# Optimization experiments

Hardware: AMD Instinct MI355X
Metric: run time of the kernel (lower is better)

Reference implementation:

```python
import jax, jax.numpy as jnp
import numpy as np

N = 16384
E = 524288
C = 16

def setup_inputs() -> dict:
    key = jax.random.key(0)
    ks = jax.random.split(key, 8)
    x = jax.random.normal(ks[0], (N, N), dtype=jnp.float32)
    edge_index = jax.random.randint(ks[1], (2, E), 0, N, dtype=jnp.int64)
    def glorot(k, fi, fo):
        s = jnp.sqrt(6.0 / (fi + fo)).astype(jnp.float32)
        return jax.random.uniform(k, (fi, fo), jnp.float32, -s, s)
    return {
        "x": x,
        "edge_index": edge_index,
        "W1": glorot(ks[2], N, 64),  "b1": jnp.zeros((64,), jnp.float32),
        "W2": glorot(ks[3], 64, 32), "b2": jnp.zeros((32,), jnp.float32),
        "W3": glorot(ks[4], 32, C),  "b3": jnp.zeros((C,), jnp.float32),
    }

def _gcn_norm(edge_index, n):
    # add self loops, compute symmetric normalization (PyG gcn_norm)
    loops = jnp.arange(n, dtype=edge_index.dtype)
    row = jnp.concatenate([edge_index[0], loops])  # source
    col = jnp.concatenate([edge_index[1], loops])  # target (aggregation index)
    deg = jax.ops.segment_sum(jnp.ones_like(col, dtype=jnp.float32), col, num_segments=n)
    dis = jnp.where(deg > 0, jax.lax.rsqrt(deg), 0.0)
    norm = dis[row] * dis[col]  # [E+N]
    return row, col, norm

def _gcn_conv(h, row, col, norm, W, b, n):
    h = h @ W                              # [N, F_out]
    msg = h[row] * norm[:, None]           # gather + scale per edge
    out = jax.ops.segment_sum(msg, col, num_segments=n)  # scatter-add at targets
    return out + b

def reference(x, edge_index, W1, b1, W2, b2, W3, b3):
    n = x.shape[0]
    row, col, norm = _gcn_norm(edge_index, n)
    h = jax.nn.relu(_gcn_conv(x, row, col, norm, W1, b1, n))
    h = jax.nn.relu(_gcn_conv(h, row, col, norm, W2, b2, n))
    h = _gcn_conv(h, row, col, norm, W3, b3, n)
    return jax.nn.softmax(h, axis=1)
```

## Files before the change

### kernel.cpp

```cpp
#include <hip/hip_runtime.h>


typedef __attribute__((ext_vector_type(8))) short bf16x8;
typedef __attribute__((ext_vector_type(4))) float f32x4;
typedef __attribute__((ext_vector_type(4))) float fv4;

__device__ __forceinline__ float4 ldnt4(const float* p) {
    fv4 v = __builtin_nontemporal_load((const fv4*)p);
    return make_float4(v.x, v.y, v.z, v.w);
}
__device__ __forceinline__ void stnt(float* p, float v) {
    __builtin_nontemporal_store(v, p);
}

__device__ __forceinline__ unsigned cvt_pk_bf16(float a, float b) {
    unsigned r;
    asm("v_cvt_pk_bf16_f32 %0, %1, %2" : "=v"(r) : "v"(a), "v"(b));
    return r;
}

__device__ __forceinline__ void lds_barrier() {
    asm volatile("s_waitcnt lgkmcnt(0)" ::: "memory");
    __builtin_amdgcn_s_barrier();
    asm volatile("" ::: "memory");
}

__device__ __forceinline__ unsigned short f2bf_rne(float f) {
    unsigned u = __float_as_uint(f);
    unsigned r = (u + 0x7FFFu + ((u >> 16) & 1u)) >> 16;
    return (unsigned short)r;
}

__global__ void init_prep_k(const int* __restrict__ ei, int* __restrict__ flag,
                            int* __restrict__ cnt, int n,
                            const float* __restrict__ W1,
                            unsigned short* __restrict__ Bt, int K) {
    int t = blockIdx.x * blockDim.x + threadIdx.x;
    if (t < n) cnt[t] = 0;
    if (t == 0) {
        int f = 1;
        for (int i = 0; i < 256; ++i) {
            if (ei[2 * i + 1] != 0) { f = 0; break; }
        }
        *flag = f;
    }
    if (t < K * 64) {
        int nn = t & 63, k = t >> 6;
        float f = W1[(size_t)k * 64 + nn];
        unsigned short hi = f2bf_rne(f);
        float hf = __uint_as_float((unsigned)hi << 16);
        unsigned short lo = f2bf_rne(f - hf);
        Bt[(size_t)nn * K + k] = hi;
        Bt[(size_t)64 * K + (size_t)nn * K + k] = lo;
    }
}

__device__ __forceinline__ int edge_val(const int* __restrict__ ei, long long idx, int f64) {
    return f64 ? ei[2 * idx] : ei[(int)idx];
}

__global__ void count_deg_k(const int* __restrict__ ei, int E, const int* __restrict__ flag,
                            int* __restrict__ cnt) {
    int e = blockIdx.x * blockDim.x + threadIdx.x;
    if (e >= E) return;
    int f = *flag;
    int c = edge_val(ei, (long long)E + e, f);
    atomicAdd(&cnt[c], 1);
}

__global__ void scan_blk_k(const int* __restrict__ cnt, int* __restrict__ offs,
                           float* __restrict__ dis, int* __restrict__ cursor,
                           int* __restrict__ btot, int n) {
    __shared__ int sh[256];
    const int t = threadIdx.x;
    const int idx = blockIdx.x * 256 + t;
    int v = (idx < n) ? cnt[idx] : 0;
    sh[t] = v;
    __syncthreads();
    for (int o = 1; o < 256; o <<= 1) {
        int add = (t >= o) ? sh[t - o] : 0;
        __syncthreads();
        sh[t] += add;
        __syncthreads();
    }
    if (idx < n) {
        offs[idx] = sh[t] - v;
        cursor[idx] = 0;
        dis[idx] = rsqrtf((float)(v + 1));
    }
    if (t == 255) btot[blockIdx.x] = sh[255];
}

__global__ void scan_add_k(int* __restrict__ offs, const int* __restrict__ btot,
                           int n, int nb) {
    __shared__ int base_sh, tot_sh;
    const int t = threadIdx.x;
    if (t == 0) {
        int base = 0, tot = 0;
        for (int i = 0; i < nb; ++i) {
            int v = btot[i];
            if (i < (int)blockIdx.x) base += v;
            tot += v;
        }
        base_sh = base;
        tot_sh = tot;
    }
    __syncthreads();
    int idx = blockIdx.x * 256 + t;
    if (idx < n) offs[idx] += base_sh;
    if (blockIdx.x == 0 && t == 0) offs[n] = tot_sh;
}

__global__ void fill_csr_k(const int* __restrict__ ei, int E, const int* __restrict__ flag,
                           const int* __restrict__ offs, int* __restrict__ cursor,
                           const float* __restrict__ dis, int* __restrict__ src,
                           float* __restrict__ w) {
    int e = blockIdx.x * blockDim.x + threadIdx.x;
    if (e >= E) return;
    int f = *flag;
    int r = edge_val(ei, (long long)e, f);
    int c = edge_val(ei, (long long)E + e, f);
    int pos = offs[c] + atomicAdd(&cursor[c], 1);
    src[pos] = r;
    w[pos] = dis[r] * dis[c];
}

__global__ __launch_bounds__(256) void gemm1_mfma_k(
    const float* __restrict__ A, const unsigned short* __restrict__ Bt,
    float* __restrict__ P, int n, int K, int kchunk) {
    __shared__ unsigned short As[2][128][40];
    const int tid = threadIdx.x;
    const int lane = tid & 63;
    const int wid = tid >> 6;
    const int wm = wid >> 1, wn = wid & 1;
    const int lrow = lane & 15, lkh = lane >> 4;
    const int bid = blockIdx.x;
    const int by = (bid & 7) >> 1;
    const int bx = ((bid >> 3) << 1) | (bid & 1);
    const int bm = bx * 128;
    const int k0 = by * kchunk;
    const int iters = kchunk / 32;

    const unsigned short* Bh = Bt;
    const unsigned short* Bl = Bt + (size_t)64 * K;

    f32x4 acc[4][2] = {};
    float4 st[4];

    auto loadA = [&](int kt) {
#pragma unroll
        for (int i = 0; i < 4; ++i) {
            int v = tid + i * 256;
            int r = v >> 3, c = (v & 7) * 4;
            st[i] = ldnt4(A + (size_t)(bm + r) * K + k0 + kt * 32 + c);
        }
    };

    loadA(0);
    for (int kt = 0; kt < iters; ++kt) {
        bf16x8 bh[2], bl[2];
#pragma unroll
        for (int nf = 0; nf < 2; ++nf) {
            int brow = wn * 32 + nf * 16 + lrow;
            size_t bo = (size_t)brow * K + k0 + kt * 32 + lkh * 8;
            bh[nf] = *(const bf16x8*)(Bh + bo);
            bl[nf] = *(const bf16x8*)(Bl + bo);
        }
#pragma unroll
        for (int i = 0; i < 4; ++i) {
            int v = tid + i * 256;
            int r = v >> 3, c = (v & 7) * 4;
            float f0 = st[i].x, f1 = st[i].y, f2 = st[i].z, f3 = st[i].w;
            unsigned h01 = cvt_pk_bf16(f0, f1);
            unsigned h23 = cvt_pk_bf16(f2, f3);
            float r0 = f0 - __uint_as_float(h01 << 16);
            float r1 = f1 - __uint_as_float(h01 & 0xFFFF0000u);
            float r2 = f2 - __uint_as_float(h23 << 16);
            float r3 = f3 - __uint_as_float(h23 & 0xFFFF0000u);
            unsigned l01 = cvt_pk_bf16(r0, r1);
            unsigned l23 = cvt_pk_bf16(r2, r3);
            *(uint2*)&As[0][r][c] = make_uint2(h01, h23);
            *(uint2*)&As[1][r][c] = make_uint2(l01, l23);
        }
        lds_barrier();
        if (kt + 1 < iters) loadA(kt + 1);
        bf16x8 ah[4], al[4];
#pragma unroll
        for (int mf = 0; mf < 4; ++mf) {
            int row = wm * 64 + mf * 16 + lrow;
            ah[mf] = *(const bf16x8*)&As[0][row][lkh * 8];
            al[mf] = *(const bf16x8*)&As[1][row][lkh * 8];
        }
#pragma unroll
        for (int mf = 0; mf < 4; ++mf)
#pragma unroll
            for (int nf = 0; nf < 2; ++nf) {
                acc[mf][nf] = __builtin_amdgcn_mfma_f32_16x16x32_bf16(ah[mf], bh[nf], acc[mf][nf], 0, 0, 0);
                acc[mf][nf] = __builtin_amdgcn_mfma_f32_16x16x32_bf16(al[mf], bh[nf], acc[mf][nf], 0, 0, 0);
                acc[mf][nf] = __builtin_amdgcn_mfma_f32_16x16x32_bf16(ah[mf], bl[nf], acc[mf][nf], 0, 0, 0);
            }
        lds_barrier();
    }
    float* out = P + (size_t)by * n * 64;
#pragma unroll
    for (int mf = 0; mf < 4; ++mf)
#pragma unroll
        for (int nf = 0; nf < 2; ++nf)
#pragma unroll
            for (int j = 0; j < 4; ++j) {
                int row = bm + wm * 64 + mf * 16 + lkh * 4 + j;
                int col = wn * 32 + nf * 16 + lrow;
                stnt(out + (size_t)row * 64 + col, acc[mf][nf][j]);
            }
}

__global__ void reduce4_k(float4* __restrict__ p, size_t q) {
    size_t i = (size_t)blockIdx.x * blockDim.x + threadIdx.x;
    if (i >= q) return;
    float4 a = p[i];
#pragma unroll
    for (int z = 1; z < 4; ++z) {
        float4 b = ldnt4((const float*)(p + i + (size_t)z * q));
        a.x += b.x; a.y += b.y; a.z += b.z; a.w += b.w;
    }
    p[i] = a;
}

__global__ __launch_bounds__(256) void prop64_gemm2_k(
    const float* __restrict__ h, const int* __restrict__ offs,
    const int* __restrict__ src, const float* __restrict__ w,
    const float* __restrict__ dis, const float* __restrict__ b1,
    const float* __restrict__ W2, float* __restrict__ H2a, int n) {
    __shared__ float Ws[64 * 32];
    __shared__ float rows[16][68];
    const int tid = threadIdx.x;
    for (int i = tid; i < 64 * 32; i += 256) Ws[i] = W2[i];
    const int t = blockIdx.x * 256 + tid;
    const int node = t >> 4, q = t & 15, nl = tid >> 4;
    float4 acc = make_float4(0.f, 0.f, 0.f, 0.f);
    int p0 = offs[node], p1 = offs[node + 1];
    for (int p = p0; p < p1; ++p) {
        float ww = w[p];
        float4 hv = *(const float4*)(h + (size_t)src[p] * 64 + q * 4);
        acc.x = fmaf(ww, hv.x, acc.x);
        acc.y = fmaf(ww, hv.y, acc.y);
        acc.z = fmaf(ww, hv.z, acc.z);
        acc.w = fmaf(ww, hv.w, acc.w);
    }
    float d = dis[node];
    float ds = d * d;
    float4 hv = *(const float4*)(h + (size_t)node * 64 + q * 4);
    float4 bv = *(const float4*)(b1 + q * 4);
    acc.x = fmaxf(fmaf(ds, hv.x, acc.x) + bv.x, 0.f);
    acc.y = fmaxf(fmaf(ds, hv.y, acc.y) + bv.y, 0.f);
    acc.z = fmaxf(fmaf(ds, hv.z, acc.z) + bv.z, 0.f);
    acc.w = fmaxf(fmaf(ds, hv.w, acc.w) + bv.w, 0.f);
    *(float4*)&rows[nl][q * 4] = acc;
    __syncthreads();
    const int c0 = q * 2;
    float s0 = 0.f, s1 = 0.f;
#pragma unroll
    for (int k = 0; k < 64; ++k) {
        float v = rows[nl][k];
        s0 = fmaf(v, Ws[k * 32 + c0], s0);
        s1 = fmaf(v, Ws[k * 32 + c0 + 1], s1);
    }
    H2a[(size_t)node * 32 + c0] = s0;
    H2a[(size_t)node * 32 + c0 + 1] = s1;
}

__global__ __launch_bounds__(256) void prop32_gemm3_k(
    const float* __restrict__ h, const int* __restrict__ offs,
    const int* __restrict__ src, const float* __restrict__ w,
    const float* __restrict__ dis, const float* __restrict__ b2,
    const float* __restrict__ W3, float* __restrict__ H3a, int n) {
    __shared__ float Ws[32 * 16];
    __shared__ float rows[32][36];
    const int tid = threadIdx.x;
    for (int i = tid; i < 32 * 16; i += 256) Ws[i] = W3[i];
    const int t = blockIdx.x * 256 + tid;
    const int node = t >> 3, q = t & 7, nl = tid >> 3;
    float4 acc = make_float4(0.f, 0.f, 0.f, 0.f);
    int p0 = offs[node], p1 = offs[node + 1];
    for (int p = p0; p < p1; ++p) {
        float ww = w[p];
        float4 hv = *(const float4*)(h + (size_t)src[p] * 32 + q * 4);
        acc.x = fmaf(ww, hv.x, acc.x);
        acc.y = fmaf(ww, hv.y, acc.y);
        acc.z = fmaf(ww, hv.z, acc.z);
        acc.w = fmaf(ww, hv.w, acc.w);
    }
    float d = dis[node];
    float ds = d * d;
    float4 hv = *(const float4*)(h + (size_t)node * 32 + q * 4);
    float4 bv = *(const float4*)(b2 + q * 4);
    acc.x = fmaxf(fmaf(ds, hv.x, acc.x) + bv.x, 0.f);
    acc.y = fmaxf(fmaf(ds, hv.y, acc.y) + bv.y, 0.f);
    acc.z = fmaxf(fmaf(ds, hv.z, acc.z) + bv.z, 0.f);
    acc.w = fmaxf(fmaf(ds, hv.w, acc.w) + bv.w, 0.f);
    *(float4*)&rows[nl][q * 4] = acc;
    __syncthreads();
    const int c0 = q * 2;
    float s0 = 0.f, s1 = 0.f;
#pragma unroll
    for (int k = 0; k < 32; ++k) {
        float v = rows[nl][k];
        s0 = fmaf(v, Ws[k * 16 + c0], s0);
        s1 = fmaf(v, Ws[k * 16 + c0 + 1], s1);
    }
    H3a[(size_t)node * 16 + c0] = s0;
    H3a[(size_t)node * 16 + c0 + 1] = s1;
}

__global__ void prop_softmax_k(const float* __restrict__ h, const int* __restrict__ offs,
                               const int* __restrict__ src, const float* __restrict__ w,
                               const float* __restrict__ dis, const float* __restrict__ b,
                               float* __restrict__ out, int n) {
    int t = blockIdx.x * blockDim.x + threadIdx.x;
    int node = t >> 2, q = t & 3;
    if (node >= n) return;
    float4 acc = make_float4(0.f, 0.f, 0.f, 0.f);
    int p0 = offs[node], p1 = offs[node + 1];
    for (int p = p0; p < p1; ++p) {
        float ww = w[p];
        float4 hv = *(const float4*)(h + (size_t)src[p] * 16 + q * 4);
        acc.x = fmaf(ww, hv.x, acc.x);
        acc.y = fmaf(ww, hv.y, acc.y);
        acc.z = fmaf(ww, hv.z, acc.z);
        acc.w = fmaf(ww, hv.w, acc.w);
    }
    float d = dis[node];
    float ds = d * d;
    float4 hv = *(const float4*)(h + (size_t)node * 16 + q * 4);
    float4 bv = *(const float4*)(b + q * 4);
    acc.x = fmaf(ds, hv.x, acc.x) + bv.x;
    acc.y = fmaf(ds, hv.y, acc.y) + bv.y;
    acc.z = fmaf(ds, hv.z, acc.z) + bv.z;
    acc.w = fmaf(ds, hv.w, acc.w) + bv.w;
    float m = fmaxf(fmaxf(acc.x, acc.y), fmaxf(acc.z, acc.w));
    m = fmaxf(m, __shfl_xor(m, 1));
    m = fmaxf(m, __shfl_xor(m, 2));
    float4 e;
    e.x = __expf(acc.x - m);
    e.y = __expf(acc.y - m);
    e.z = __expf(acc.z - m);
    e.w = __expf(acc.w - m);
    float s = e.x + e.y + e.z + e.w;
    s += __shfl_xor(s, 1);
    s += __shfl_xor(s, 2);
    float inv = 1.f / s;
    e.x *= inv; e.y *= inv; e.z *= inv; e.w *= inv;
    *(float4*)(out + (size_t)node * 16 + q * 4) = e;
}

extern "C" void kernel_launch(void* const* d_in, const int* in_sizes, int n_in,
                              void* d_out, int out_size, void* d_ws, size_t ws_size,
                              hipStream_t stream) {
    const float* x  = (const float*)d_in[0];
    const int*   ei = (const int*)d_in[1];
    const float* W1 = (const float*)d_in[2];
    const float* b1 = (const float*)d_in[3];
    const float* W2 = (const float*)d_in[4];
    const float* b2 = (const float*)d_in[5];
    const float* W3 = (const float*)d_in[6];
    const float* b3 = (const float*)d_in[7];
    float* out = (float*)d_out;

    const int n = in_sizes[2] / 64;
    const int K = in_sizes[0] / n;
    const int E = in_sizes[1] / 2;
    const int nb = (n + 255) / 256;

    char* ws = (char*)d_ws;
    size_t off = 0;
    auto alloc = [&](size_t bytes) {
        char* p = ws + off;
        off = (off + bytes + 255) & ~(size_t)255;
        return p;
    };
    int*   flag   = (int*)  alloc(4);
    int*   cnt    = (int*)  alloc((size_t)n * 4);
    int*   cursor = (int*)  alloc((size_t)n * 4);
    int*   offs   = (int*)  alloc((size_t)(n + 1) * 4);
    int*   btot   = (int*)  alloc((size_t)nb * 4);
    float* dis    = (float*)alloc((size_t)n * 4);
    int*   csrs   = (int*)  alloc((size_t)E * 4);
    float* csrw   = (float*)alloc((size_t)E * 4);
    unsigned short* Btw = (unsigned short*)alloc((size_t)2 * 64 * K * 2);
    float* P      = (float*)alloc((size_t)4 * n * 64 * 4);
    float* H2a    = (float*)alloc((size_t)n * 32 * 4);
    float* H3a    = (float*)alloc((size_t)n * 16 * 4);
    (void)ws_size; (void)n_in; (void)out_size;

    init_prep_k<<<(K * 64 + 255) / 256, 256, 0, stream>>>(ei, flag, cnt, n, W1, Btw, K);
    count_deg_k<<<(E + 255) / 256, 256, 0, stream>>>(ei, E, flag, cnt);
    scan_blk_k<<<nb, 256, 0, stream>>>(cnt, offs, dis, cursor, btot, n);
    scan_add_k<<<nb, 256, 0, stream>>>(offs, btot, n, nb);
    fill_csr_k<<<(E + 255) / 256, 256, 0, stream>>>(ei, E, flag, offs, cursor, dis, csrs, csrw);

    gemm1_mfma_k<<<(n / 128) * 4, 256, 0, stream>>>(x, Btw, P, n, K, K / 4);
    size_t q = (size_t)n * 64 / 4;
    reduce4_k<<<(int)((q + 255) / 256), 256, 0, stream>>>((float4*)P, q);

    prop64_gemm2_k<<<n * 16 / 256, 256, 0, stream>>>(P, offs, csrs, csrw, dis, b1, W2, H2a, n);
    prop32_gemm3_k<<<n * 8 / 256, 256, 0, stream>>>(H2a, offs, csrs, csrw, dis, b2, W3, H3a, n);
    prop_softmax_k<<<n * 4 / 256, 256, 0, stream>>>(H3a, offs, csrs, csrw, dis, b3, out, n);
}
```

Baseline: 365.3 us.

## Split degree counters into four replicas and pack CSR source/weight records

Degree counting and CSR fill now spread their atomics over four replicated counter arrays indexed by edge id mod 4, which cuts contention on hot target nodes. A per-replica base offset array is built in the scan step, so the separate cursor array is no longer needed. CSR source index and edge weight are packed into one 8-byte record, so each propagation step does one load per edge instead of two. In exchange the counter arrays take four times the memory, the scans read four times as much, and init_prep_k must now zero 4n counters, which only works if its grid has at least 4n threads.

```diff
diff --git a/kernel.cpp b/kernel.cpp
--- a/kernel.cpp
+++ b/kernel.cpp
@@ -36,7 +36,7 @@
                             const float* __restrict__ W1,
                             unsigned short* __restrict__ Bt, int K) {
     int t = blockIdx.x * blockDim.x + threadIdx.x;
-    if (t < n) cnt[t] = 0;
+    if (t < 4 * n) cnt[t] = 0;
     if (t == 0) {
         int f = 1;
         for (int i = 0; i < 256; ++i) {
@@ -60,21 +60,24 @@
 }
 
 __global__ void count_deg_k(const int* __restrict__ ei, int E, const int* __restrict__ flag,
-                            int* __restrict__ cnt) {
+                            int* __restrict__ cnt, int n) {
     int e = blockIdx.x * blockDim.x + threadIdx.x;
     if (e >= E) return;
     int f = *flag;
     int c = edge_val(ei, (long long)E + e, f);
-    atomicAdd(&cnt[c], 1);
+    atomicAdd(&cnt[(e & 3) * n + c], 1);
 }
 
 __global__ void scan_blk_k(const int* __restrict__ cnt, int* __restrict__ offs,
-                           float* __restrict__ dis, int* __restrict__ cursor,
-                           int* __restrict__ btot, int n) {
+                           float* __restrict__ dis, int* __restrict__ btot, int n) {
     __shared__ int sh[256];
     const int t = threadIdx.x;
     const int idx = blockIdx.x * 256 + t;
-    int v = (idx < n) ? cnt[idx] : 0;
+    int v = 0;
+    if (idx < n) {
+#pragma unroll
+        for (int r = 0; r < 4; ++r) v += cnt[r * n + idx];
+    }
     sh[t] = v;
     __syncthreads();
     for (int o = 1; o < 256; o <<= 1) {
@@ -85,13 +88,13 @@
     }
     if (idx < n) {
         offs[idx] = sh[t] - v;
-        cursor[idx] = 0;
         dis[idx] = rsqrtf((float)(v + 1));
     }
     if (t == 255) btot[blockIdx.x] = sh[255];
 }
 
 __global__ void scan_add_k(int* __restrict__ offs, const int* __restrict__ btot,
+                           const int* __restrict__ cnt, int* __restrict__ base4,
                            int n, int nb) {
     __shared__ int base_sh, tot_sh;
     const int t = threadIdx.x;
@@ -107,22 +110,32 @@
     }
     __syncthreads();
     int idx = blockIdx.x * 256 + t;
-    if (idx < n) offs[idx] += base_sh;
+    if (idx < n) {
+        int o = offs[idx] + base_sh;
+        offs[idx] = o;
+        int b = o;
+#pragma unroll
+        for (int r = 0; r < 4; ++r) {
+            base4[r * n + idx] = b;
+            b += cnt[r * n + idx];
+        }
+    }
     if (blockIdx.x == 0 && t == 0) offs[n] = tot_sh;
 }
 
 __global__ void fill_csr_k(const int* __restrict__ ei, int E, const int* __restrict__ flag,
-                           const int* __restrict__ offs, int* __restrict__ cursor,
-                           const float* __restrict__ dis, int* __restrict__ src,
-                           float* __restrict__ w) {
+                           int* __restrict__ base4,
+                           const float* __restrict__ dis,
+                           unsigned long long* __restrict__ csr8, int n) {
     int e = blockIdx.x * blockDim.x + threadIdx.x;
     if (e >= E) return;
     int f = *flag;
     int r = edge_val(ei, (long long)e, f);
     int c = edge_val(ei, (long long)E + e, f);
-    int pos = offs[c] + atomicAdd(&cursor[c], 1);
-    src[pos] = r;
-    w[pos] = dis[r] * dis[c];
+    int pos = atomicAdd(&base4[(e & 3) * n + c], 1);
+    float w = dis[r] * dis[c];
+    unsigned long long rec = ((unsigned long long)__float_as_uint(w) << 32) | (unsigned)r;
+    csr8[pos] = rec;
 }
 
 __global__ __launch_bounds__(256) void gemm1_mfma_k(
@@ -228,7 +241,7 @@
 
 __global__ __launch_bounds__(256) void prop64_gemm2_k(
     const float* __restrict__ h, const int* __restrict__ offs,
-    const int* __restrict__ src, const float* __restrict__ w,
+    const int2* __restrict__ csr8,
     const float* __restrict__ dis, const float* __restrict__ b1,
     const float* __restrict__ W2, float* __restrict__ H2a, int n) {
     __shared__ float Ws[64 * 32];
@@ -240,8 +253,9 @@
     float4 acc = make_float4(0.f, 0.f, 0.f, 0.f);
     int p0 = offs[node], p1 = offs[node + 1];
     for (int p = p0; p < p1; ++p) {
-        float ww = w[p];
-        float4 hv = *(const float4*)(h + (size_t)src[p] * 64 + q * 4);
+        int2 rec = csr8[p];
+        float ww = __int_as_float(rec.y);
+        float4 hv = *(const float4*)(h + (size_t)rec.x * 64 + q * 4);
         acc.x = fmaf(ww, hv.x, acc.x);
         acc.y = fmaf(ww, hv.y, acc.y);
         acc.z = fmaf(ww, hv.z, acc.z);
@@ -271,7 +285,7 @@
 
 __global__ __launch_bounds__(256) void prop32_gemm3_k(
     const float* __restrict__ h, const int* __restrict__ offs,
-    const int* __restrict__ src, const float* __restrict__ w,
+    const int2* __restrict__ csr8,
     const float* __restrict__ dis, const float* __restrict__ b2,
     const float* __restrict__ W3, float* __restrict__ H3a, int n) {
     __shared__ float Ws[32 * 16];
@@ -283,8 +297,9 @@
     float4 acc = make_float4(0.f, 0.f, 0.f, 0.f);
     int p0 = offs[node], p1 = offs[node + 1];
     for (int p = p0; p < p1; ++p) {
-        float ww = w[p];
-        float4 hv = *(const float4*)(h + (size_t)src[p] * 32 + q * 4);
+        int2 rec = csr8[p];
+        float ww = __int_as_float(rec.y);
+        float4 hv = *(const float4*)(h + (size_t)rec.x * 32 + q * 4);
         acc.x = fmaf(ww, hv.x, acc.x);
         acc.y = fmaf(ww, hv.y, acc.y);
         acc.z = fmaf(ww, hv.z, acc.z);
@@ -313,7 +328,7 @@
 }
 
 __global__ void prop_softmax_k(const float* __restrict__ h, const int* __restrict__ offs,
-                               const int* __restrict__ src, const float* __restrict__ w,
+                               const int2* __restrict__ csr8,
                                const float* __restrict__ dis, const float* __restrict__ b,
                                float* __restrict__ out, int n) {
     int t = blockIdx.x * blockDim.x + threadIdx.x;
@@ -322,8 +337,9 @@
     float4 acc = make_float4(0.f, 0.f, 0.f, 0.f);
     int p0 = offs[node], p1 = offs[node + 1];
     for (int p = p0; p < p1; ++p) {
-        float ww = w[p];
-        float4 hv = *(const float4*)(h + (size_t)src[p] * 16 + q * 4);
+        int2 rec = csr8[p];
+        float ww = __int_as_float(rec.y);
+        float4 hv = *(const float4*)(h + (size_t)rec.x * 16 + q * 4);
         acc.x = fmaf(ww, hv.x, acc.x);
         acc.y = fmaf(ww, hv.y, acc.y);
         acc.z = fmaf(ww, hv.z, acc.z);
@@ -379,13 +395,12 @@
         return p;
     };
     int*   flag   = (int*)  alloc(4);
-    int*   cnt    = (int*)  alloc((size_t)n * 4);
-    int*   cursor = (int*)  alloc((size_t)n * 4);
+    int*   cnt    = (int*)  alloc((size_t)4 * n * 4);
+    int*   base4  = (int*)  alloc((size_t)4 * n * 4);
     int*   offs   = (int*)  alloc((size_t)(n + 1) * 4);
     int*   btot   = (int*)  alloc((size_t)nb * 4);
     float* dis    = (float*)alloc((size_t)n * 4);
-    int*   csrs   = (int*)  alloc((size_t)E * 4);
-    float* csrw   = (float*)alloc((size_t)E * 4);
+    unsigned long long* csr8 = (unsigned long long*)alloc((size_t)E * 8);
     unsigned short* Btw = (unsigned short*)alloc((size_t)2 * 64 * K * 2);
     float* P      = (float*)alloc((size_t)4 * n * 64 * 4);
     float* H2a    = (float*)alloc((size_t)n * 32 * 4);
@@ -393,16 +408,16 @@
     (void)ws_size; (void)n_in; (void)out_size;
 
     init_prep_k<<<(K * 64 + 255) / 256, 256, 0, stream>>>(ei, flag, cnt, n, W1, Btw, K);
-    count_deg_k<<<(E + 255) / 256, 256, 0, stream>>>(ei, E, flag, cnt);
-    scan_blk_k<<<nb, 256, 0, stream>>>(cnt, offs, dis, cursor, btot, n);
-    scan_add_k<<<nb, 256, 0, stream>>>(offs, btot, n, nb);
-    fill_csr_k<<<(E + 255) / 256, 256, 0, stream>>>(ei, E, flag, offs, cursor, dis, csrs, csrw);
+    count_deg_k<<<(E + 255) / 256, 256, 0, stream>>>(ei, E, flag, cnt, n);
+    scan_blk_k<<<nb, 256, 0, stream>>>(cnt, offs, dis, btot, n);
+    scan_add_k<<<nb, 256, 0, stream>>>(offs, btot, cnt, base4, n, nb);
+    fill_csr_k<<<(E + 255) / 256, 256, 0, stream>>>(ei, E, flag, base4, dis, csr8, n);
 
     gemm1_mfma_k<<<(n / 128) * 4, 256, 0, stream>>>(x, Btw, P, n, K, K / 4);
     size_t q = (size_t)n * 64 / 4;
     reduce4_k<<<(int)((q + 255) / 256), 256, 0, stream>>>((float4*)P, q);
 
-    prop64_gemm2_k<<<n * 16 / 256, 256, 0, stream>>>(P, offs, csrs, csrw, dis, b1, W2, H2a, n);
-    prop32_gemm3_k<<<n * 8 / 256, 256, 0, stream>>>(H2a, offs, csrs, csrw, dis, b2, W3, H3a, n);
-    prop_softmax_k<<<n * 4 / 256, 256, 0, stream>>>(H3a, offs, csrs, csrw, dis, b3, out, n);
-}
+    prop64_gemm2_k<<<n * 16 / 256, 256, 0, stream>>>(P, offs, (const int2*)csr8, dis, b1, W2, H2a, n);
+    prop32_gemm3_k<<<n * 8 / 256, 256, 0, stream>>>(H2a, offs, (const int2*)csr8, dis, b2, W3, H3a, n);
+    prop_softmax_k<<<n * 4 / 256, 256, 0, stream>>>(H3a, offs, (const int2*)csr8, dis, b3, out, n);
+}
```

Result: faster. 355.4 us (-2.7%).
